# Optimization experiments

Measured on AMD Instinct MI355X. Metric: run time of the kernel, lower is better.

The kernel has to match this reference:

```python
import jax, jax.numpy as jnp
import numpy as np

B, L, D_IN, D, DEPTH, H = 1, 4095, 1536, 768, 4, 12
HD = D // H
FFN = 4 * D
GRID = 128
TILE = 256
SEGMENTS = (1024, 2048, 4096, 8192, 16384)
RATIOS = (1, 2, 4, 8, 16)
EPS = 1e-5
NEG = -1e9


def _sincos_1d(d, pos):
    omega = 1.0 / (10000.0 ** (np.arange(d // 2, dtype=np.float64) / (d / 2.0)))
    out = np.einsum('m,d->md', pos.reshape(-1).astype(np.float64), omega)
    return np.concatenate([np.sin(out), np.cos(out)], axis=1)


def _pos_embed_2d(d, g):
    # MAE-style 2d sincos grid; row index = coords[...,0], col = coords[...,1]
    gw, gh = np.meshgrid(np.arange(g, dtype=np.float64), np.arange(g, dtype=np.float64))
    emb_h = _sincos_1d(d // 2, gw)
    emb_w = _sincos_1d(d // 2, gh)
    pe = np.concatenate([emb_h, emb_w], axis=1)  # [g*g, d]
    return np.concatenate([np.zeros((1, d)), pe], axis=0).astype(np.float32)  # cls row


def setup_inputs() -> dict:
    key = jax.random.key(0)
    ks = jax.random.split(key, 16)
    n = lambda k, sh: 0.02 * jax.random.normal(k, sh, jnp.float32)
    x = jax.random.normal(ks[0], (B, L, D_IN), jnp.float32)
    coords = jax.random.uniform(ks[1], (B, L, 2), jnp.float32, 0.0, float(GRID * TILE))
    return {
        'x': x,
        'coords': coords,
        'pos_embed': jnp.asarray(_pos_embed_2d(D, GRID)),
        'cls_token': n(ks[2], (1, 1, D)),
        'patch_w': n(ks[3], (D_IN, D)),
        'patch_b': jnp.zeros((D,), jnp.float32),
        'ln1_g': jnp.ones((DEPTH, D), jnp.float32),
        'ln1_b': jnp.zeros((DEPTH, D), jnp.float32),
        'wq': n(ks[4], (DEPTH, D, D)), 'bq': jnp.zeros((DEPTH, D), jnp.float32),
        'wk': n(ks[5], (DEPTH, D, D)), 'bk': jnp.zeros((DEPTH, D), jnp.float32),
        'wv': n(ks[6], (DEPTH, D, D)), 'bv': jnp.zeros((DEPTH, D), jnp.float32),
        'wo': n(ks[7], (DEPTH, D, D)), 'bo': jnp.zeros((DEPTH, D), jnp.float32),
        'ln2_g': jnp.ones((DEPTH, D), jnp.float32),
        'ln2_b': jnp.zeros((DEPTH, D), jnp.float32),
        'w1': n(ks[8], (DEPTH, D, FFN)), 'b1': jnp.zeros((DEPTH, FFN), jnp.float32),
        'w2': n(ks[9], (DEPTH, FFN, D)), 'b2': jnp.zeros((DEPTH, D), jnp.float32),
        'enc_ln_g': jnp.ones((D,), jnp.float32),
        'enc_ln_b': jnp.zeros((D,), jnp.float32),
        'norm_g': jnp.ones((D,), jnp.float32),
        'norm_b': jnp.zeros((D,), jnp.float32),
    }


def _ln(t, g, b):
    m = t.mean(-1, keepdims=True)
    v = ((t - m) ** 2).mean(-1, keepdims=True)
    return (t - m) * jax.lax.rsqrt(v + EPS) * g + b


def _branch(q, k, v, w, r):
    # One LongNet dilated branch: segments of length w, per-head dilation r.
    Bq, S, Hh, hd = q.shape
    Lp = ((S + w - 1) // w) * w
    pad = Lp - S
    if pad:
        q = jnp.pad(q, ((0, 0), (0, pad), (0, 0), (0, 0)))
        k = jnp.pad(k, ((0, 0), (0, pad), (0, 0), (0, 0)))
        v = jnp.pad(v, ((0, 0), (0, pad), (0, 0), (0, 0)))
    n = Lp // w
    m = w // r
    # head-dependent offset subsampling (offset = head % r)
    idx = (jnp.arange(Hh) % r)[:, None] + r * jnp.arange(m)[None, :]  # [H, m]

    def seg(t):
        t = t.reshape(Bq, n, w, Hh, hd).transpose(0, 1, 3, 2, 4)  # [B,n,H,w,hd]
        return jnp.take_along_axis(t, idx[None, None, :, :, None], axis=3)  # [B,n,H,m,hd]

    qs, ks, vs = seg(q), seg(k), seg(v)
    valid = (jnp.arange(n)[:, None, None] * w + idx[None]) < S  # [n,H,m] key validity
    s = jnp.einsum('bnhqd,bnhkd->bnhqk', qs, ks)
    s = jnp.where(valid[None, :, :, None, :], s, NEG)
    lse_s = jax.scipy.special.logsumexp(s, axis=-1)              # [B,n,H,m]
    o_s = jnp.einsum('bnhqk,bnhkd->bnhqd', jax.nn.softmax(s, axis=-1), vs)
    hix = jnp.arange(Hh)[:, None]
    out = jnp.zeros((Bq, n, Hh, w, hd), q.dtype).at[:, :, hix, idx].set(o_s)
    lse = jnp.full((Bq, n, Hh, w), NEG, q.dtype).at[:, :, hix, idx].set(lse_s)
    out = out.transpose(0, 1, 3, 2, 4).reshape(Bq, Lp, Hh, hd)[:, :S]
    lse = lse.transpose(0, 1, 3, 2).reshape(Bq, Lp, Hh)[:, :S]
    return out, lse


def _forward(x, coords, pos_embed, cls_token, patch_w, patch_b, ln1_g, ln1_b,
             wq, bq, wk, bk, wv, bv, wo, bo, ln2_g, ln2_b, w1, b1, w2, b2,
             enc_ln_g, enc_ln_b, norm_g, norm_b):
    h = x @ patch_w + patch_b  # PatchEmbed (norm_layer=None -> Identity)
    c = jnp.floor(coords / TILE)
    pos = (c[..., 0] * GRID + c[..., 1]).astype(jnp.int32) + 1  # [B,L]
    h = h + pos_embed[pos]
    cls = jnp.broadcast_to(cls_token + pos_embed[0], (h.shape[0], 1, D))
    h = jnp.concatenate([cls, h], axis=1)  # [B, S, D], S = L+1
    S = h.shape[1]

    def layer(hcur, p):
        g1, bb1, wq_, bq_, wk_, bk_, wv_, bv_, wo_, bo_, g2, bb2, wf1, bf1, wf2, bf2 = p
        t = _ln(hcur, g1, bb1)
        q = (t @ wq_ + bq_).reshape(B, S, H, HD) * (HD ** -0.5)
        k = (t @ wk_ + bk_).reshape(B, S, H, HD)
        v = (t @ wv_ + bv_).reshape(B, S, H, HD)
        outs, lses = [], []
        for w_, r_ in zip(SEGMENTS, RATIOS):
            o, l = _branch(q, k, v, w_, r_)
            outs.append(o)
            lses.append(l)
        # LongNet combine: branches weighted by their softmax denominators
        wts = jax.nn.softmax(jnp.stack(lses), axis=0)  # [nb,B,S,H]
        attn = (wts[..., None] * jnp.stack(outs)).sum(0).reshape(B, S, D)
        hcur = hcur + attn @ wo_ + bo_
        t = _ln(hcur, g2, bb2)
        hcur = hcur + jax.nn.gelu(t @ wf1 + bf1) @ wf2 + bf2
        return hcur, None

    h, _ = jax.lax.scan(layer, h, (ln1_g, ln1_b, wq, bq, wk, bk, wv, bv,
                                   wo, bo, ln2_g, ln2_b, w1, b1, w2, b2))
    h = _ln(h, enc_ln_g, enc_ln_b)  # encoder final LN (normalize_before)
    h = _ln(h, norm_g, norm_b)      # module self.norm
    return h[:, 0]                  # cls token (global_pool=False)


def reference(x, coords, pos_embed, cls_token, patch_w, patch_b, ln1_g, ln1_b,
              wq, bq, wk, bk, wv, bv, wo, bo, ln2_g, ln2_b, w1, b1, w2, b2,
              enc_ln_g, enc_ln_b, norm_g, norm_b):
    return _forward(x, coords, pos_embed, cls_token, patch_w, patch_b, ln1_g, ln1_b,
                    wq, bq, wk, bk, wv, bv, wo, bo, ln2_g, ln2_b, w1, b1, w2, b2,
                    enc_ln_g, enc_ln_b, norm_g, norm_b)
```

## Files before the change

### kernel.cpp

```cpp
#include <hip/hip_runtime.h>
#include <hip/hip_bf16.h>
#include <math.h>
#include <stdint.h>

#define S_LEN 4096
#define L_LEN 4095
#define DIN   1536
#define DM    768
#define NHEAD 12
#define HDIM  64
#define FFND  3072
#define NEGV  (-1e9f)
#define EPS   1e-5f

typedef unsigned short u16;
typedef unsigned int   u32;
typedef short short8 __attribute__((ext_vector_type(8)));
typedef float f32x4 __attribute__((ext_vector_type(4)));
typedef float f32x16 __attribute__((ext_vector_type(16)));
typedef int i32x2 __attribute__((ext_vector_type(2)));

__device__ __forceinline__ u16 f2b(float f) {
    union { float f; u32 u; } x; x.f = f;
    u32 r = (x.u + 0x7FFF + ((x.u >> 16) & 1)) >> 16;
    return (u16)r;
}
__device__ __forceinline__ float b2f(u16 v) {
    union { u32 u; float f; } x; x.u = ((u32)v) << 16;
    return x.f;
}
__device__ __forceinline__ float gelu_tanh(float x) {
    float x3 = x * x * x;
    return 0.5f * x * (1.f + tanhf(0.7978845608f * (x + 0.044715f * x3)));
}
__device__ __forceinline__ float block_reduce_sum(float v, float* sbuf) {
#pragma unroll
    for (int o = 32; o > 0; o >>= 1) v += __shfl_down(v, o, 64);
    __syncthreads();
    if ((threadIdx.x & 63) == 0) sbuf[threadIdx.x >> 6] = v;
    __syncthreads();
    return sbuf[0] + sbuf[1] + sbuf[2] + sbuf[3];
}
__device__ __forceinline__ void gload16(const void* g, void* l) {
    __builtin_amdgcn_global_load_lds((const __attribute__((address_space(1))) void*)g,
                                     (__attribute__((address_space(3))) void*)l,
                                     16, 0, 0);
}
__device__ __forceinline__ void lds_barrier() {
    asm volatile("s_waitcnt lgkmcnt(0)" ::: "memory");
    __builtin_amdgcn_s_barrier();
    __builtin_amdgcn_sched_barrier(0);
}

template <int BM, int BN>
__device__ __forceinline__ void gemm_bt(
    const u16* __restrict__ A, const u16* __restrict__ Bt,
    const float* __restrict__ bias, const float* __restrict__ res,
    float* __restrict__ outf, u16* __restrict__ outb,
    int M, int N, int K, float scale, int dogelu, int bx, int by)
{
    constexpr int MI = BM / 32;
    constexpr int NI = BN / 32;
    constexpr int AI = BM / 32;
    constexpr int BI = BN / 32;
    __shared__ u16 As[BM * 64];
    __shared__ u16 Bs[BN * 64];
    const int tid = threadIdx.x, wv = tid >> 6, l = tid & 63;
    const int bm = by * BM, bn = bx * BN;
    const int wm = wv >> 1, wn = wv & 1;

    f32x4 acc[MI][NI];
#pragma unroll
    for (int i = 0; i < MI; ++i)
#pragma unroll
        for (int j = 0; j < NI; ++j) acc[i][j] = (f32x4){0.f, 0.f, 0.f, 0.f};

    for (int k0 = 0; k0 < K; k0 += 64) {
#pragma unroll
        for (int i = 0; i < AI; ++i) {
            int row = (wv * AI + i) * 8 + (l >> 3);
            int col = ((l & 7) ^ (row & 7)) * 8;
            int grow = bm + row; if (grow > M - 1) grow = M - 1;
            gload16(A + (size_t)grow * K + k0 + col, &As[(wv * AI + i) * 512]);
        }
#pragma unroll
        for (int i = 0; i < BI; ++i) {
            int row = (wv * BI + i) * 8 + (l >> 3);
            int col = ((l & 7) ^ (row & 7)) * 8;
            gload16(Bt + (size_t)(bn + row) * K + k0 + col, &Bs[(wv * BI + i) * 512]);
        }
        __syncthreads();
#pragma unroll
        for (int kc = 0; kc < 2; ++kc) {
            short8 a[MI], b[NI];
#pragma unroll
            for (int mi = 0; mi < MI; ++mi) {
                int row = wm * (BM / 2) + mi * 16 + (l & 15);
                int off = ((l >> 4) * 16 + kc * 64) ^ ((row & 7) << 4);
                a[mi] = *(const short8*)&As[(row * 128 + off) >> 1];
            }
#pragma unroll
            for (int ni = 0; ni < NI; ++ni) {
                int row = wn * (BN / 2) + ni * 16 + (l & 15);
                int off = ((l >> 4) * 16 + kc * 64) ^ ((row & 7) << 4);
                b[ni] = *(const short8*)&Bs[(row * 128 + off) >> 1];
            }
#pragma unroll
            for (int mi = 0; mi < MI; ++mi)
#pragma unroll
                for (int ni = 0; ni < NI; ++ni)
                    acc[mi][ni] = __builtin_amdgcn_mfma_f32_16x16x32_bf16(
                        a[mi], b[ni], acc[mi][ni], 0, 0, 0);
        }
        __syncthreads();
    }
#pragma unroll
    for (int mi = 0; mi < MI; ++mi) {
#pragma unroll
        for (int rg = 0; rg < 4; ++rg) {
            int row = bm + wm * (BM / 2) + mi * 16 + (l >> 4) * 4 + rg;
            if (row >= M) continue;
#pragma unroll
            for (int ni = 0; ni < NI; ++ni) {
                int col = bn + wn * (BN / 2) + ni * 16 + (l & 15);
                float v = (acc[mi][ni][rg] + bias[col]) * scale;
                if (dogelu) v = gelu_tanh(v);
                if (res) v += res[(size_t)row * N + col];
                if (outf) outf[(size_t)row * N + col] = v;
                if (outb) outb[(size_t)row * N + col] = f2b(v);
            }
        }
    }
}

__global__ __launch_bounds__(256) void gemm128_kernel(
    const u16* __restrict__ A, const u16* __restrict__ Bt,
    const float* __restrict__ bias, const float* __restrict__ res,
    float* __restrict__ outf, u16* __restrict__ outb,
    int M, int N, int K, float scale, int dogelu)
{
    gemm_bt<128, 128>(A, Bt, bias, res, outf, outb, M, N, K, scale, dogelu,
                      blockIdx.x, blockIdx.y);
}
__global__ __launch_bounds__(256) void gemm6464_kernel(
    const u16* __restrict__ A, const u16* __restrict__ Bt,
    const float* __restrict__ bias, const float* __restrict__ res,
    float* __restrict__ outf, u16* __restrict__ outb,
    int M, int N, int K, float scale, int dogelu)
{
    gemm_bt<64, 64>(A, Bt, bias, res, outf, outb, M, N, K, scale, dogelu,
                    blockIdx.x, blockIdx.y);
}
__global__ __launch_bounds__(256) void qkv_kernel(
    const u16* __restrict__ t,
    const u16* __restrict__ wqT, const u16* __restrict__ wkT, const u16* __restrict__ wvT,
    const float* __restrict__ bq, const float* __restrict__ bk, const float* __restrict__ bv,
    u16* __restrict__ q, u16* __restrict__ k, u16* __restrict__ v)
{
    int z = blockIdx.z;
    const u16* B = (z == 0) ? wqT : (z == 1) ? wkT : wvT;
    const float* bias = (z == 0) ? bq : (z == 1) ? bk : bv;
    u16* C = (z == 0) ? q : (z == 1) ? k : v;
    float scale = (z == 0) ? 0.125f * 1.4426950408889634f : 1.0f;
    gemm_bt<128, 128>(t, B, bias, nullptr, nullptr, C, S_LEN, DM, DM, scale, 0,
                      blockIdx.x, blockIdx.y);
}

__global__ __launch_bounds__(256) void transpose_cvt(
    const float* __restrict__ s0, const float* __restrict__ s1,
    const float* __restrict__ s2, const float* __restrict__ s3,
    u16* __restrict__ dst, int K, int N)
{
    int z = blockIdx.z;
    const float* src = (z == 0) ? s0 : (z == 1) ? s1 : (z == 2) ? s2 : s3;
    u16* d = dst + (size_t)z * K * N;
    __shared__ float tile[64][65];
    const int t = threadIdx.x;
    const int tk = blockIdx.y * 64, tn = blockIdx.x * 64;
    const int r0 = t >> 4, c0 = (t & 15) * 4;
#pragma unroll
    for (int i = 0; i < 4; ++i) {
        const float* sp = &src[(size_t)(tk + r0 + i * 16) * N + tn + c0];
        tile[r0 + i * 16][c0 + 0] = sp[0];
        tile[r0 + i * 16][c0 + 1] = sp[1];
        tile[r0 + i * 16][c0 + 2] = sp[2];
        tile[r0 + i * 16][c0 + 3] = sp[3];
    }
    __syncthreads();
#pragma unroll
    for (int i = 0; i < 4; ++i) {
        int nr = r0 + i * 16;
        u32 lo = (u32)f2b(tile[c0 + 0][nr]) | ((u32)f2b(tile[c0 + 1][nr]) << 16);
        u32 hi = (u32)f2b(tile[c0 + 2][nr]) | ((u32)f2b(tile[c0 + 3][nr]) << 16);
        *(uint2*)&d[(size_t)(tn + nr) * K + tk + c0] = make_uint2(lo, hi);
    }
}

__global__ __launch_bounds__(256) void prep_weights(
    const float* __restrict__ wq, const float* __restrict__ wk,
    const float* __restrict__ wv, const float* __restrict__ wo,
    const float* __restrict__ w1, const float* __restrict__ w2,
    u16* __restrict__ wTdd, u16* __restrict__ w1T, u16* __restrict__ w2T)
{
    __shared__ float tile[64][65];
    const int id = blockIdx.x;
    const float* src; u16* dst; int K, N, tk64, tn64;
    if (id < 576) {
        int z = id / 144, rm = id % 144;
        src = (z == 0) ? wq : (z == 1) ? wk : (z == 2) ? wv : wo;
        dst = wTdd + (size_t)z * DM * DM;
        K = DM; N = DM; tk64 = rm / 12; tn64 = rm % 12;
    } else if (id < 1152) {
        int rm = id - 576;
        src = w1; dst = w1T; K = DM; N = FFND; tk64 = rm / 48; tn64 = rm % 48;
    } else {
        int rm = id - 1152;
        src = w2; dst = w2T; K = FFND; N = DM; tk64 = rm / 12; tn64 = rm % 12;
    }
    const int t = threadIdx.x;
    const int tk = tk64 * 64, tn = tn64 * 64;
    const int r0 = t >> 4, c0 = (t & 15) * 4;
#pragma unroll
    for (int i = 0; i < 4; ++i) {
        const float* sp = &src[(size_t)(tk + r0 + i * 16) * N + tn + c0];
        tile[r0 + i * 16][c0 + 0] = sp[0];
        tile[r0 + i * 16][c0 + 1] = sp[1];
        tile[r0 + i * 16][c0 + 2] = sp[2];
        tile[r0 + i * 16][c0 + 3] = sp[3];
    }
    __syncthreads();
#pragma unroll
    for (int i = 0; i < 4; ++i) {
        int nr = r0 + i * 16;
        u32 lo = (u32)f2b(tile[c0 + 0][nr]) | ((u32)f2b(tile[c0 + 1][nr]) << 16);
        u32 hi = (u32)f2b(tile[c0 + 2][nr]) | ((u32)f2b(tile[c0 + 3][nr]) << 16);
        *(uint2*)&dst[(size_t)(tn + nr) * K + tk + c0] = make_uint2(lo, hi);
    }
}

__global__ __launch_bounds__(256) void cvt_bf16_kernel(
    const float* __restrict__ x, u16* __restrict__ xb, int n4)
{
    int stride = gridDim.x * 256;
    for (int i = blockIdx.x * 256 + threadIdx.x; i < n4; i += stride) {
        float4 v = ((const float4*)x)[i];
        u32 lo = (u32)f2b(v.x) | ((u32)f2b(v.y) << 16);
        u32 hi = (u32)f2b(v.z) | ((u32)f2b(v.w) << 16);
        ((uint2*)xb)[i] = make_uint2(lo, hi);
    }
}

__global__ __launch_bounds__(192) void ln_kernel(
    const float* __restrict__ in, u16* __restrict__ out,
    const float* __restrict__ g, const float* __restrict__ b)
{
    __shared__ float sA[3], sB[3];
    const int s = blockIdx.x, tid = threadIdx.x;
    float4 x = ((const float4*)(in + (size_t)s * DM))[tid];
    float sum = x.x + x.y + x.z + x.w;
#pragma unroll
    for (int o = 32; o > 0; o >>= 1) sum += __shfl_down(sum, o, 64);
    if ((tid & 63) == 0) sA[tid >> 6] = sum;
    __syncthreads();
    float m = (sA[0] + sA[1] + sA[2]) * (1.f / DM);
    float dx = x.x - m, dy = x.y - m, dz = x.z - m, dw = x.w - m;
    float vs = dx * dx + dy * dy + dz * dz + dw * dw;
#pragma unroll
    for (int o = 32; o > 0; o >>= 1) vs += __shfl_down(vs, o, 64);
    if ((tid & 63) == 0) sB[tid >> 6] = vs;
    __syncthreads();
    float rs = rsqrtf((sB[0] + sB[1] + sB[2]) * (1.f / DM) + EPS);
    float4 gv = ((const float4*)g)[tid];
    float4 bv = ((const float4*)b)[tid];
    u32 lo = (u32)f2b(dx * rs * gv.x + bv.x) | ((u32)f2b(dy * rs * gv.y + bv.y) << 16);
    u32 hi = (u32)f2b(dz * rs * gv.z + bv.z) | ((u32)f2b(dw * rs * gv.w + bv.w) << 16);
    ((uint2*)(out + (size_t)s * DM))[tid] = make_uint2(lo, hi);
}

__global__ __launch_bounds__(256) void posadd_kernel(
    float* __restrict__ h, const float* __restrict__ coords,
    const float* __restrict__ pe, const float* __restrict__ cls)
{
    const int s = blockIdx.x;
    const int tid = threadIdx.x;
    if (s == 0) {
        for (int c = tid; c < DM; c += 256) h[c] = cls[c] + pe[c];
    } else {
        float c0 = floorf(coords[(size_t)(s - 1) * 2 + 0] * (1.f / 256.f));
        float c1 = floorf(coords[(size_t)(s - 1) * 2 + 1] * (1.f / 256.f));
        int pos = (int)(c0 * 128.f + c1) + 1;
        float* hr = h + (size_t)s * DM;
        const float* pr = pe + (size_t)pos * DM;
        for (int c = tid; c < DM; c += 256) hr[c] += pr[c];
    }
}

__global__ __launch_bounds__(256, 3) void attn_kernel(
    const u16* __restrict__ qb, const u16* __restrict__ kbuf, const u16* __restrict__ vb,
    u16* __restrict__ obuf, u16* __restrict__ tp, float* __restrict__ lse)
{
    __shared__ u16 Vt[2][64 * 64];
    __shared__ float dbuf[4][32];

    const int tid = threadIdx.x, wv = tid >> 6, l = tid & 63;
    const int lq = l & 31, lh = l >> 5;
    const int bid = blockIdx.x;
    int b, half = 0, qtile, head, seg = 0;
    if (bid < 768) {
        b = 0; int i = bid; half = i & 1; qtile = (i >> 1) & 7;
        int rest = i >> 4; head = rest % 12; seg = rest / 12;
    } else if (bid < 1152) {
        b = 1; int i = bid - 768; half = i & 1; qtile = (i >> 1) & 7;
        int rest = i >> 4; head = rest % 12; seg = rest / 12;
    } else if (bid < 1344) {
        b = 2; int i = bid - 1152; half = i & 1; qtile = (i >> 1) & 7;
        head = i >> 4;
    } else if (bid < 1392) {
        b = 3; int i = bid - 1344; qtile = i & 3; head = i >> 2;
    } else {
        b = 4; int i = bid - 1392; qtile = i & 1; head = i >> 1;
    }
    const int slot = (b < 3) ? b * 2 + half : 3 + b;
    const int r = 1 << b;
    const int w = 1024 << b;
    const int keyoff = (b < 3) ? half * 512 : 0;
    const int ntiles = (b == 4) ? 4 : 8;
    const size_t base = (size_t)seg * w + (head & (r - 1));
    const int q0 = qtile * 128 + wv * 32;
    const size_t kstep = (size_t)r * DM;

    const size_t sq_l = base + (size_t)r * (q0 + lq);
    const u16* qp = qb + sq_l * DM + head * 64 + lh * 8;
    short8 qf[4];
#pragma unroll
    for (int s = 0; s < 4; ++s) qf[s] = *(const short8*)(qp + s * 16);

    const u16* kp = kbuf + (base + (size_t)r * (keyoff + lq)) * DM + head * 64 + lh * 8;
    const int c = tid & 7, pp = tid >> 3;
    const u16* vsrc = vb + (base + (size_t)r * (keyoff + 2 * pp)) * DM + head * 64 + c * 8;

#define VPACK(dstbuf, A8, B8) do {                                          \
    _Pragma("unroll") for (int j = 0; j < 8; ++j) {                         \
        int i_ = (j + c) & 7; int hd_ = c * 8 + i_;                         \
        u32 val_ = (u32)(u16)(A8)[i_] | ((u32)(u16)(B8)[i_] << 16);         \
        int byte_ = hd_ * 128 + ((pp * 4) ^ (i_ << 4));                     \
        *(u32*)&Vt[dstbuf][byte_ >> 1] = val_; } } while (0)

    f32x16 oacc0 = {0.f,0.f,0.f,0.f,0.f,0.f,0.f,0.f,0.f,0.f,0.f,0.f,0.f,0.f,0.f,0.f};
    f32x16 oacc1 = oacc0;
    float mw = -INFINITY, dl = 0.f;

    short8 van = *(const short8*)vsrc;
    short8 vbn = *(const short8*)(vsrc + kstep);
    VPACK(0, van, vbn);
    van = *(const short8*)(vsrc + 64 * kstep);
    vbn = *(const short8*)(vsrc + 65 * kstep);
    short8 kf[8];
#pragma unroll
    for (int s = 0; s < 4; ++s) {
        kf[s]     = *(const short8*)(kp + s * 16);
        kf[4 + s] = *(const short8*)(kp + 32 * kstep + s * 16);
    }
    lds_barrier();

    for (int t = 0; t < ntiles; ++t) {
        const int curb = t & 1;
        f32x16 s0 = {0.f,0.f,0.f,0.f,0.f,0.f,0.f,0.f,0.f,0.f,0.f,0.f,0.f,0.f,0.f,0.f};
        f32x16 s1 = s0;
#pragma unroll
        for (int s = 0; s < 4; ++s)
            s0 = __builtin_amdgcn_mfma_f32_32x32x16_bf16(kf[s], qf[s], s0, 0, 0, 0);
#pragma unroll
        for (int s = 0; s < 4; ++s)
            s1 = __builtin_amdgcn_mfma_f32_32x32x16_bf16(kf[4 + s], qf[s], s1, 0, 0, 0);

        if (t + 1 < ntiles) {
            const u16* kn = kp + (size_t)(t + 1) * 64 * kstep;
#pragma unroll
            for (int s = 0; s < 4; ++s) {
                kf[s]     = *(const short8*)(kn + s * 16);
                kf[4 + s] = *(const short8*)(kn + 32 * kstep + s * 16);
            }
        }

        float pm[16];
#pragma unroll
        for (int i = 0; i < 16; ++i) pm[i] = fmaxf(s0[i], s1[i]);
#pragma unroll
        for (int i = 0; i < 8; ++i) pm[i] = fmaxf(pm[i], pm[i + 8]);
#pragma unroll
        for (int i = 0; i < 4; ++i) pm[i] = fmaxf(pm[i], pm[i + 4]);
        float mloc = fmaxf(fmaxf(pm[0], pm[1]), fmaxf(pm[2], pm[3]));
        if (__any(mloc > mw + 8.f)) {
            float mn = mloc;
#pragma unroll
            for (int o = 1; o < 64; o <<= 1) mn = fmaxf(mn, __shfl_xor(mn, o, 64));
            float al = exp2f(mw - mn);
            mw = mn;
            dl *= al;
#pragma unroll
            for (int i = 0; i < 16; ++i) { oacc0[i] *= al; oacc1[i] *= al; }
        }
        float ds = 0.f;
#pragma unroll
        for (int i = 0; i < 16; ++i) { s0[i] = exp2f(s0[i] - mw); ds += s0[i]; }
#pragma unroll
        for (int i = 0; i < 16; ++i) { s1[i] = exp2f(s1[i] - mw); ds += s1[i]; }
        ds += __shfl_xor(ds, 32, 64);
        dl += ds;

        if (t + 1 < ntiles) VPACK(curb ^ 1, van, vbn);
        if (t + 2 < ntiles) {
            van = *(const short8*)(vsrc + (size_t)(t + 2) * 64 * kstep);
            vbn = *(const short8*)(vsrc + ((size_t)(t + 2) * 64 + 1) * kstep);
        }

#pragma unroll
        for (int kb2 = 0; kb2 < 2; ++kb2) {
            u32 wd[8];
#pragma unroll
            for (int j = 0; j < 8; ++j) {
                float lo = (kb2 == 0) ? s0[2 * j] : s1[2 * j];
                float hi = (kb2 == 0) ? s0[2 * j + 1] : s1[2 * j + 1];
                asm("v_cvt_pk_bf16_f32 %0, %1, %2" : "=v"(wd[j]) : "v"(lo), "v"(hi));
            }
#pragma unroll
            for (int ks2 = 0; ks2 < 2; ++ks2) {
                i32x2 X = __builtin_amdgcn_permlane32_swap(
                    (int)wd[ks2 * 4 + 0], (int)wd[ks2 * 4 + 2], false, false);
                i32x2 Y = __builtin_amdgcn_permlane32_swap(
                    (int)wd[ks2 * 4 + 1], (int)wd[ks2 * 4 + 3], false, false);
                union { u32 u[4]; short8 s; } pk;
                pk.u[0] = (u32)X[0]; pk.u[1] = (u32)Y[0];
                pk.u[2] = (u32)X[1]; pk.u[3] = (u32)Y[1];
                const int tt = kb2 * 2 + ks2;
#pragma unroll
                for (int hg = 0; hg < 2; ++hg) {
                    int row = hg * 32 + lq;
                    int byteoff = row * 128 + ((lh * 16 + tt * 32) ^ ((row & 7) << 4));
                    short8 vf = *(const short8*)&Vt[curb][byteoff >> 1];
                    if (hg == 0)
                        oacc0 = __builtin_amdgcn_mfma_f32_32x32x16_bf16(pk.s, vf, oacc0, 0, 0, 0);
                    else
                        oacc1 = __builtin_amdgcn_mfma_f32_32x32x16_bf16(pk.s, vf, oacc1, 0, 0, 0);
                }
            }
        }
        lds_barrier();
    }

    if (l < 32) dbuf[wv][lq] = dl;
    u16* ob = (slot == 7) ? tp : obuf + (size_t)slot * S_LEN * DM;
    float* lse_b = lse + (size_t)slot * S_LEN * NHEAD;
    if (l < 32) lse_b[sq_l * NHEAD + head] = mw + log2f(dl);
#pragma unroll
    for (int reg = 0; reg < 16; ++reg) {
        int qloc = (reg & 3) + 8 * (reg >> 2) + 4 * lh;
        float invd = 1.f / dbuf[wv][qloc];
        size_t sq = base + (size_t)r * (q0 + qloc);
        u16* orow = ob + sq * DM + head * 64;
        u32 pk2;
        float v0 = oacc0[reg] * invd, v1 = oacc1[reg] * invd;
        asm("v_cvt_pk_bf16_f32 %0, %1, %2" : "=v"(pk2) : "v"(v0), "v"(v1));
        orow[lq]      = (u16)(pk2 & 0xffff);
        orow[32 + lq] = (u16)(pk2 >> 16);
    }
#undef VPACK
}

__global__ __launch_bounds__(192) void combine_kernel(
    const u16* __restrict__ obuf, const float* __restrict__ lse,
    u16* __restrict__ t)
{
    const int s = blockIdx.x;
    const int tid = threadIdx.x;
    const int c0 = tid * 4, head = c0 >> 6;
    const size_t SD = (size_t)S_LEN * DM;
    const size_t SN = (size_t)S_LEN * NHEAD;
    const bool v6 = ((s ^ head) & 7) == 0;
    const bool v7 = (s & 15) == head;
    float lv[8];
#pragma unroll
    for (int b = 0; b < 6; ++b)
        lv[b] = lse[b * SN + (size_t)s * NHEAD + head];
    lv[6] = v6 ? lse[6 * SN + (size_t)s * NHEAD + head] : NEGV;
    lv[7] = v7 ? lse[7 * SN + (size_t)s * NHEAD + head] : NEGV;
    float mx = lv[0];
#pragma unroll
    for (int b = 1; b < 8; ++b) mx = fmaxf(mx, lv[b]);
    float wsum = 0.f, o0 = 0.f, o1 = 0.f, o2 = 0.f, o3 = 0.f;
#pragma unroll
    for (int b = 0; b < 8; ++b) {
        bool valid = (b < 6) | (b == 6 && v6) | (b == 7 && v7);
        if (valid) {
            float wb = exp2f(lv[b] - mx);
            wsum += wb;
            const u16* src = (b == 7) ? t : obuf + (size_t)b * SD;
            uint2 u = *(const uint2*)(src + (size_t)s * DM + c0);
            o0 += wb * b2f((u16)(u.x & 0xffff));
            o1 += wb * b2f((u16)(u.x >> 16));
            o2 += wb * b2f((u16)(u.y & 0xffff));
            o3 += wb * b2f((u16)(u.y >> 16));
        }
    }
    float inv = 1.f / wsum;
    u32 lo = (u32)f2b(o0 * inv) | ((u32)f2b(o1 * inv) << 16);
    u32 hi = (u32)f2b(o2 * inv) | ((u32)f2b(o3 * inv) << 16);
    ((uint2*)(t + (size_t)s * DM))[tid] = make_uint2(lo, hi);
}

__global__ __launch_bounds__(256) void final_ln_kernel(
    const float* __restrict__ h,
    const float* __restrict__ g1, const float* __restrict__ b1,
    const float* __restrict__ g2, const float* __restrict__ b2,
    float* __restrict__ out)
{
    __shared__ float sbuf[4];
    const int tid = threadIdx.x;
    float x0 = h[tid], x1 = h[tid + 256], x2 = h[tid + 512];
    float m = block_reduce_sum(x0 + x1 + x2, sbuf) * (1.f / DM);
    float d0 = x0 - m, d1 = x1 - m, d2 = x2 - m;
    float var = block_reduce_sum(d0 * d0 + d1 * d1 + d2 * d2, sbuf) * (1.f / DM);
    float rs = rsqrtf(var + EPS);
    float y0 = d0 * rs * g1[tid]       + b1[tid];
    float y1 = d1 * rs * g1[tid + 256] + b1[tid + 256];
    float y2 = d2 * rs * g1[tid + 512] + b1[tid + 512];
    m = block_reduce_sum(y0 + y1 + y2, sbuf) * (1.f / DM);
    d0 = y0 - m; d1 = y1 - m; d2 = y2 - m;
    var = block_reduce_sum(d0 * d0 + d1 * d1 + d2 * d2, sbuf) * (1.f / DM);
    rs = rsqrtf(var + EPS);
    out[tid]       = d0 * rs * g2[tid]       + b2[tid];
    out[tid + 256] = d1 * rs * g2[tid + 256] + b2[tid + 256];
    out[tid + 512] = d2 * rs * g2[tid + 512] + b2[tid + 512];
}

extern "C" void kernel_launch(void* const* d_in, const int* in_sizes, int n_in,
                              void* d_out, int out_size, void* d_ws, size_t ws_size,
                              hipStream_t stream)
{
    (void)in_sizes; (void)n_in; (void)out_size; (void)ws_size;
    const float* x        = (const float*)d_in[0];
    const float* coords   = (const float*)d_in[1];
    const float* pos_emb  = (const float*)d_in[2];
    const float* cls_tok  = (const float*)d_in[3];
    const float* patch_w  = (const float*)d_in[4];
    const float* patch_b  = (const float*)d_in[5];
    const float* ln1_g    = (const float*)d_in[6];
    const float* ln1_b    = (const float*)d_in[7];
    const float* wq       = (const float*)d_in[8];
    const float* bq       = (const float*)d_in[9];
    const float* wk       = (const float*)d_in[10];
    const float* bk       = (const float*)d_in[11];
    const float* wv       = (const float*)d_in[12];
    const float* bv       = (const float*)d_in[13];
    const float* wo       = (const float*)d_in[14];
    const float* bo       = (const float*)d_in[15];
    const float* ln2_g    = (const float*)d_in[16];
    const float* ln2_b    = (const float*)d_in[17];
    const float* w1       = (const float*)d_in[18];
    const float* b1       = (const float*)d_in[19];
    const float* w2       = (const float*)d_in[20];
    const float* b2       = (const float*)d_in[21];
    const float* enc_g    = (const float*)d_in[22];
    const float* enc_b    = (const float*)d_in[23];
    const float* norm_g   = (const float*)d_in[24];
    const float* norm_b   = (const float*)d_in[25];
    float* out = (float*)d_out;

    const size_t SD = (size_t)S_LEN * DM;
    const size_t DD = (size_t)DM * DM;
    const size_t DF = (size_t)DM * FFND;
    const size_t SN = (size_t)S_LEN * NHEAD;

    char* p = (char*)d_ws;
    float* h   = (float*)p;              p += SD * 4;
    u16* t     = (u16*)p;                p += SD * 2;
    u16* qb    = (u16*)p;                p += SD * 2;
    u16* kb    = (u16*)p;                p += SD * 2;
    u16* vb    = (u16*)p;                p += SD * 2;
    float* lse = (float*)p;              p += 8 * SN * 4;
    u16* obuf  = (u16*)p;                p += 7 * SD * 2;
    u16* ffn   = obuf;
    u16* xb    = obuf;
    u16* pwT   = (u16*)p;                p += (size_t)DIN * DM * 2;
    u16* wTdd  = (u16*)p;                p += 4 * DD * 2;
    u16* w1T   = (u16*)p;                p += DF * 2;
    u16* w2T   = (u16*)p;                p += DF * 2;

    cvt_bf16_kernel<<<2048, 256, 0, stream>>>(x, xb, (L_LEN * DIN) / 4);
    transpose_cvt<<<dim3(DM / 64, DIN / 64, 1), 256, 0, stream>>>(
        patch_w, patch_w, patch_w, patch_w, pwT, DIN, DM);
    gemm6464_kernel<<<dim3(DM / 64, 64), 256, 0, stream>>>(
        xb, pwT, patch_b, nullptr, h + DM, nullptr, L_LEN, DM, DIN, 1.f, 0);
    posadd_kernel<<<S_LEN, 256, 0, stream>>>(h, coords, pos_emb, cls_tok);

    for (int l = 0; l < 4; ++l) {
        const size_t lDD = (size_t)l * DD;
        const size_t lDF = (size_t)l * DF;
        prep_weights<<<1728, 256, 0, stream>>>(
            wq + lDD, wk + lDD, wv + lDD, wo + lDD, w1 + lDF, w2 + lDF,
            wTdd, w1T, w2T);

        ln_kernel<<<S_LEN, 192, 0, stream>>>(h, t, ln1_g + l * DM, ln1_b + l * DM);
        qkv_kernel<<<dim3(6, 32, 3), 256, 0, stream>>>(
            t, wTdd, wTdd + DD, wTdd + 2 * DD,
            bq + l * DM, bk + l * DM, bv + l * DM, qb, kb, vb);
        attn_kernel<<<1416, 256, 0, stream>>>(qb, kb, vb, obuf, t, lse);
        combine_kernel<<<S_LEN, 192, 0, stream>>>(obuf, lse, t);
        gemm6464_kernel<<<dim3(12, 64), 256, 0, stream>>>(
            t, wTdd + 3 * DD, bo + l * DM, h, h, nullptr, S_LEN, DM, DM, 1.f, 0);
        ln_kernel<<<S_LEN, 192, 0, stream>>>(h, t, ln2_g + l * DM, ln2_b + l * DM);
        gemm128_kernel<<<dim3(24, 32), 256, 0, stream>>>(
            t, w1T, b1 + (size_t)l * FFND, nullptr, nullptr, ffn,
            S_LEN, FFND, DM, 1.f, 1);
        gemm6464_kernel<<<dim3(12, 64), 256, 0, stream>>>(
            ffn, w2T, b2 + l * DM, h, h, nullptr, S_LEN, DM, FFND, 1.f, 0);
    }
    final_ln_kernel<<<1, 256, 0, stream>>>(h, enc_g, enc_b, norm_g, norm_b, out);
}
```

Measured before the change: 1.104 ms.

## Pre-transpose V per dilation branch and load V fragments directly from global

Adds a vtrans kernel that writes V in a per-branch, per-head transposed layout, so the attention kernel can load the PV-MMA operands straight into registers. This removes the in-kernel LDS transpose, the double buffer and the per-tile barriers. The row-sum broadcast now uses a shuffle instead of shared memory, and MFMA sections are wrapped in s_setprio. Separately, the 64x64 GEMMs (patch, out-proj, FFN2) become 128x64 tiles. The cost is an extra kernel launch per layer, about 5x the V size in extra workspace and global traffic, and fewer blocks for the N=768 GEMMs.

```diff
diff --git a/kernel.cpp b/kernel.cpp
--- a/kernel.cpp
+++ b/kernel.cpp
@@ -46,11 +46,6 @@
                                      (__attribute__((address_space(3))) void*)l,
                                      16, 0, 0);
 }
-__device__ __forceinline__ void lds_barrier() {
-    asm volatile("s_waitcnt lgkmcnt(0)" ::: "memory");
-    __builtin_amdgcn_s_barrier();
-    __builtin_amdgcn_sched_barrier(0);
-}
 
 template <int BM, int BN>
 __device__ __forceinline__ void gemm_bt(
@@ -142,14 +137,14 @@
     gemm_bt<128, 128>(A, Bt, bias, res, outf, outb, M, N, K, scale, dogelu,
                       blockIdx.x, blockIdx.y);
 }
-__global__ __launch_bounds__(256) void gemm6464_kernel(
+__global__ __launch_bounds__(256) void gemm12864_kernel(
     const u16* __restrict__ A, const u16* __restrict__ Bt,
     const float* __restrict__ bias, const float* __restrict__ res,
     float* __restrict__ outf, u16* __restrict__ outb,
     int M, int N, int K, float scale, int dogelu)
 {
-    gemm_bt<64, 64>(A, Bt, bias, res, outf, outb, M, N, K, scale, dogelu,
-                    blockIdx.x, blockIdx.y);
+    gemm_bt<128, 64>(A, Bt, bias, res, outf, outb, M, N, K, scale, dogelu,
+                     blockIdx.x, blockIdx.y);
 }
 __global__ __launch_bounds__(256) void qkv_kernel(
     const u16* __restrict__ t,
@@ -238,6 +233,48 @@
     }
 }
 
+__global__ __launch_bounds__(256) void vtrans_kernel(
+    const u16* __restrict__ vb, u16* __restrict__ vtb)
+{
+    __shared__ u16 tile[64 * 64];
+    const int t = threadIdx.x;
+    const int iblk = blockIdx.x;
+    const int head = blockIdx.y;
+    const int b = blockIdx.z;
+    const int r = 1 << b;
+    const int sr = 4096 >> b;
+    const int idx0 = iblk * 64;
+    const int c = idx0 / sr;
+    const int q0 = idx0 - c * sr;
+    {
+        const int i = t >> 2, hc = (t & 3) * 16;
+        const int pos = c + r * (q0 + i);
+        const u16* src = vb + (size_t)pos * DM + head * 64 + hc;
+        short8 a = *(const short8*)src;
+        short8 d = *(const short8*)(src + 8);
+        const int sw = (i & 7) << 4;
+        *(short8*)((char*)tile + i * 128 + ((hc * 2) ^ sw)) = a;
+        *(short8*)((char*)tile + i * 128 + (((hc * 2) + 16) ^ sw)) = d;
+    }
+    __syncthreads();
+#pragma unroll
+    for (int it = 0; it < 2; ++it) {
+        int wi = t + it * 256;
+        int hd = wi >> 3, grp = wi & 7;
+        u16 v[8];
+#pragma unroll
+        for (int j = 0; j < 8; ++j)
+            v[j] = *(const u16*)((char*)tile + (grp * 8 + j) * 128 + ((hd * 2) ^ (j << 4)));
+        uint4 o;
+        o.x = (u32)v[0] | ((u32)v[1] << 16);
+        o.y = (u32)v[2] | ((u32)v[3] << 16);
+        o.z = (u32)v[4] | ((u32)v[5] << 16);
+        o.w = (u32)v[6] | ((u32)v[7] << 16);
+        u16* dst = vtb + (((size_t)b * NHEAD + head) * 64 + hd) * S_LEN + idx0 + grp * 8;
+        *(uint4*)dst = o;
+    }
+}
+
 __global__ __launch_bounds__(256) void cvt_bf16_kernel(
     const float* __restrict__ x, u16* __restrict__ xb, int n4)
 {
@@ -296,13 +333,11 @@
 }
 
 __global__ __launch_bounds__(256, 3) void attn_kernel(
-    const u16* __restrict__ qb, const u16* __restrict__ kbuf, const u16* __restrict__ vb,
+    const u16* __restrict__ qb, const u16* __restrict__ kbuf,
+    const u16* __restrict__ vtb,
     u16* __restrict__ obuf, u16* __restrict__ tp, float* __restrict__ lse)
 {
-    __shared__ u16 Vt[2][64 * 64];
-    __shared__ float dbuf[4][32];
-
-    const int tid = threadIdx.x, wv = tid >> 6, l = tid & 63;
+    const int tid = threadIdx.x, l = tid & 63;
     const int lq = l & 31, lh = l >> 5;
     const int bid = blockIdx.x;
     int b, half = 0, qtile, head, seg = 0;
@@ -320,9 +355,11 @@
     } else {
         b = 4; int i = bid - 1392; qtile = i & 1; head = i >> 1;
     }
+    const int wv = tid >> 6;
     const int slot = (b < 3) ? b * 2 + half : 3 + b;
     const int r = 1 << b;
     const int w = 1024 << b;
+    const int sr = 4096 >> b;
     const int keyoff = (b < 3) ? half * 512 : 0;
     const int ntiles = (b == 4) ? 4 : 8;
     const size_t base = (size_t)seg * w + (head & (r - 1));
@@ -336,43 +373,37 @@
     for (int s = 0; s < 4; ++s) qf[s] = *(const short8*)(qp + s * 16);
 
     const u16* kp = kbuf + (base + (size_t)r * (keyoff + lq)) * DM + head * 64 + lh * 8;
-    const int c = tid & 7, pp = tid >> 3;
-    const u16* vsrc = vb + (base + (size_t)r * (keyoff + 2 * pp)) * DM + head * 64 + c * 8;
-
-#define VPACK(dstbuf, A8, B8) do {                                          \
-    _Pragma("unroll") for (int j = 0; j < 8; ++j) {                         \
-        int i_ = (j + c) & 7; int hd_ = c * 8 + i_;                         \
-        u32 val_ = (u32)(u16)(A8)[i_] | ((u32)(u16)(B8)[i_] << 16);         \
-        int byte_ = hd_ * 128 + ((pp * 4) ^ (i_ << 4));                     \
-        *(u32*)&Vt[dstbuf][byte_ >> 1] = val_; } } while (0)
+    const u16* vr0 = vtb + (((size_t)b * NHEAD + head) * 64 + lq) * S_LEN
+                   + (head & (r - 1)) * sr + seg * 1024 + keyoff + lh * 8;
+    const u16* vr1 = vr0 + (size_t)32 * S_LEN;
 
     f32x16 oacc0 = {0.f,0.f,0.f,0.f,0.f,0.f,0.f,0.f,0.f,0.f,0.f,0.f,0.f,0.f,0.f,0.f};
     f32x16 oacc1 = oacc0;
     float mw = -INFINITY, dl = 0.f;
 
-    short8 van = *(const short8*)vsrc;
-    short8 vbn = *(const short8*)(vsrc + kstep);
-    VPACK(0, van, vbn);
-    van = *(const short8*)(vsrc + 64 * kstep);
-    vbn = *(const short8*)(vsrc + 65 * kstep);
-    short8 kf[8];
+    short8 kf[8], vf0[4], vf1[4];
 #pragma unroll
     for (int s = 0; s < 4; ++s) {
         kf[s]     = *(const short8*)(kp + s * 16);
         kf[4 + s] = *(const short8*)(kp + 32 * kstep + s * 16);
     }
-    lds_barrier();
+#pragma unroll
+    for (int tt = 0; tt < 4; ++tt) {
+        vf0[tt] = *(const short8*)(vr0 + tt * 16);
+        vf1[tt] = *(const short8*)(vr1 + tt * 16);
+    }
 
     for (int t = 0; t < ntiles; ++t) {
-        const int curb = t & 1;
         f32x16 s0 = {0.f,0.f,0.f,0.f,0.f,0.f,0.f,0.f,0.f,0.f,0.f,0.f,0.f,0.f,0.f,0.f};
         f32x16 s1 = s0;
+        __builtin_amdgcn_s_setprio(1);
 #pragma unroll
         for (int s = 0; s < 4; ++s)
             s0 = __builtin_amdgcn_mfma_f32_32x32x16_bf16(kf[s], qf[s], s0, 0, 0, 0);
 #pragma unroll
         for (int s = 0; s < 4; ++s)
             s1 = __builtin_amdgcn_mfma_f32_32x32x16_bf16(kf[4 + s], qf[s], s1, 0, 0, 0);
+        __builtin_amdgcn_s_setprio(0);
 
         if (t + 1 < ntiles) {
             const u16* kn = kp + (size_t)(t + 1) * 64 * kstep;
@@ -409,12 +440,7 @@
         ds += __shfl_xor(ds, 32, 64);
         dl += ds;
 
-        if (t + 1 < ntiles) VPACK(curb ^ 1, van, vbn);
-        if (t + 2 < ntiles) {
-            van = *(const short8*)(vsrc + (size_t)(t + 2) * 64 * kstep);
-            vbn = *(const short8*)(vsrc + ((size_t)(t + 2) * 64 + 1) * kstep);
-        }
-
+        __builtin_amdgcn_s_setprio(1);
 #pragma unroll
         for (int kb2 = 0; kb2 < 2; ++kb2) {
             u32 wd[8];
@@ -434,29 +460,31 @@
                 pk.u[0] = (u32)X[0]; pk.u[1] = (u32)Y[0];
                 pk.u[2] = (u32)X[1]; pk.u[3] = (u32)Y[1];
                 const int tt = kb2 * 2 + ks2;
-#pragma unroll
-                for (int hg = 0; hg < 2; ++hg) {
-                    int row = hg * 32 + lq;
-                    int byteoff = row * 128 + ((lh * 16 + tt * 32) ^ ((row & 7) << 4));
-                    short8 vf = *(const short8*)&Vt[curb][byteoff >> 1];
-                    if (hg == 0)
-                        oacc0 = __builtin_amdgcn_mfma_f32_32x32x16_bf16(pk.s, vf, oacc0, 0, 0, 0);
-                    else
-                        oacc1 = __builtin_amdgcn_mfma_f32_32x32x16_bf16(pk.s, vf, oacc1, 0, 0, 0);
-                }
+                oacc0 = __builtin_amdgcn_mfma_f32_32x32x16_bf16(pk.s, vf0[tt], oacc0, 0, 0, 0);
+                oacc1 = __builtin_amdgcn_mfma_f32_32x32x16_bf16(pk.s, vf1[tt], oacc1, 0, 0, 0);
             }
         }
-        lds_barrier();
-    }
-
-    if (l < 32) dbuf[wv][lq] = dl;
+        __builtin_amdgcn_s_setprio(0);
+
+        if (t + 1 < ntiles) {
+            const u16* vn0 = vr0 + (t + 1) * 64;
+            const u16* vn1 = vr1 + (t + 1) * 64;
+#pragma unroll
+            for (int tt = 0; tt < 4; ++tt) {
+                vf0[tt] = *(const short8*)(vn0 + tt * 16);
+                vf1[tt] = *(const short8*)(vn1 + tt * 16);
+            }
+        }
+    }
+
     u16* ob = (slot == 7) ? tp : obuf + (size_t)slot * S_LEN * DM;
     float* lse_b = lse + (size_t)slot * S_LEN * NHEAD;
     if (l < 32) lse_b[sq_l * NHEAD + head] = mw + log2f(dl);
 #pragma unroll
     for (int reg = 0; reg < 16; ++reg) {
         int qloc = (reg & 3) + 8 * (reg >> 2) + 4 * lh;
-        float invd = 1.f / dbuf[wv][qloc];
+        float dq = __shfl(dl, qloc, 64);
+        float invd = 1.f / dq;
         size_t sq = base + (size_t)r * (q0 + qloc);
         u16* orow = ob + sq * DM + head * 64;
         u32 pk2;
@@ -465,7 +493,6 @@
         orow[lq]      = (u16)(pk2 & 0xffff);
         orow[32 + lq] = (u16)(pk2 >> 16);
     }
-#undef VPACK
 }
 
 __global__ __launch_bounds__(192) void combine_kernel(
@@ -578,6 +605,7 @@
     u16* qb    = (u16*)p;                p += SD * 2;
     u16* kb    = (u16*)p;                p += SD * 2;
     u16* vb    = (u16*)p;                p += SD * 2;
+    u16* vtb   = (u16*)p;                p += 5 * SD * 2;
     float* lse = (float*)p;              p += 8 * SN * 4;
     u16* obuf  = (u16*)p;                p += 7 * SD * 2;
     u16* ffn   = obuf;
@@ -590,7 +618,7 @@
     cvt_bf16_kernel<<<2048, 256, 0, stream>>>(x, xb, (L_LEN * DIN) / 4);
     transpose_cvt<<<dim3(DM / 64, DIN / 64, 1), 256, 0, stream>>>(
         patch_w, patch_w, patch_w, patch_w, pwT, DIN, DM);
-    gemm6464_kernel<<<dim3(DM / 64, 64), 256, 0, stream>>>(
+    gemm12864_kernel<<<dim3(12, 32), 256, 0, stream>>>(
         xb, pwT, patch_b, nullptr, h + DM, nullptr, L_LEN, DM, DIN, 1.f, 0);
     posadd_kernel<<<S_LEN, 256, 0, stream>>>(h, coords, pos_emb, cls_tok);
 
@@ -605,15 +633,16 @@
         qkv_kernel<<<dim3(6, 32, 3), 256, 0, stream>>>(
             t, wTdd, wTdd + DD, wTdd + 2 * DD,
             bq + l * DM, bk + l * DM, bv + l * DM, qb, kb, vb);
-        attn_kernel<<<1416, 256, 0, stream>>>(qb, kb, vb, obuf, t, lse);
+        vtrans_kernel<<<dim3(64, NHEAD, 5), 256, 0, stream>>>(vb, vtb);
+        attn_kernel<<<1416, 256, 0, stream>>>(qb, kb, vtb, obuf, t, lse);
         combine_kernel<<<S_LEN, 192, 0, stream>>>(obuf, lse, t);
-        gemm6464_kernel<<<dim3(12, 64), 256, 0, stream>>>(
+        gemm12864_kernel<<<dim3(12, 32), 256, 0, stream>>>(
             t, wTdd + 3 * DD, bo + l * DM, h, h, nullptr, S_LEN, DM, DM, 1.f, 0);
         ln_kernel<<<S_LEN, 192, 0, stream>>>(h, t, ln2_g + l * DM, ln2_b + l * DM);
         gemm128_kernel<<<dim3(24, 32), 256, 0, stream>>>(
             t, w1T, b1 + (size_t)l * FFND, nullptr, nullptr, ffn,
             S_LEN, FFND, DM, 1.f, 1);
-        gemm6464_kernel<<<dim3(12, 64), 256, 0, stream>>>(
+        gemm12864_kernel<<<dim3(12, 32), 256, 0, stream>>>(
             ffn, w2T, b2 + l * DM, h, h, nullptr, S_LEN, DM, FFND, 1.f, 0);
     }
     final_ln_kernel<<<1, 256, 0, stream>>>(h, enc_g, enc_b, norm_g, norm_b, out);
```

After: 1.306 ms. 18.3% more time.

## Compute only the CLS row in the last layer after attention

Applied to the files above, without the earlier changes.

The output only needs the CLS token, so in the final layer attention, the output projection, LN2 and the FFN are computed for row 0 only. New kernels do this: a per-head CLS attention that combines the dilated branches, and a row GEMV for the projections. This removes most of the last layer's attention and GEMM work, and K/V are still computed in full for all rows. The risk is correctness if the branch validity and dilation logic for row 0 does not exactly match the full kernel's semantics.

```diff
diff --git a/kernel.cpp b/kernel.cpp
--- a/kernel.cpp
+++ b/kernel.cpp
@@ -507,6 +507,118 @@
     u32 lo = (u32)f2b(o0 * inv) | ((u32)f2b(o1 * inv) << 16);
     u32 hi = (u32)f2b(o2 * inv) | ((u32)f2b(o3 * inv) << 16);
     ((uint2*)(t + (size_t)s * DM))[tid] = make_uint2(lo, hi);
+}
+
+__global__ __launch_bounds__(256) void cls_attn_kernel(
+    const u16* __restrict__ qb, const u16* __restrict__ kb,
+    const u16* __restrict__ vb, u16* __restrict__ t)
+{
+    __shared__ float q0[64];
+    __shared__ float sc[1024];
+    __shared__ float red4[4];
+    __shared__ float po[256];
+    __shared__ float obr[5][64];
+    __shared__ float lseb[5];
+    const int head = blockIdx.x, tid = threadIdx.x;
+    if (tid < 64) q0[tid] = b2f(qb[head * 64 + tid]);
+    __syncthreads();
+
+    for (int b = 0; b < 5; ++b) {
+        const int r = 1 << b;
+        const bool valid = (head & (r - 1)) == 0;
+        if (!valid) {
+            if (tid == 0) lseb[b] = NEGV;
+            __syncthreads();
+            continue;
+        }
+        const int nv = (b < 3) ? 1024 : (b == 3 ? 512 : 256);
+        const int nit = nv >> 8;
+        float smax = -1e30f;
+        for (int it = 0; it < nit; ++it) {
+            int j = tid + it * 256;
+            const u16* kp = kb + (size_t)j * r * DM + head * 64;
+            float acc = 0.f;
+#pragma unroll
+            for (int d8 = 0; d8 < 8; ++d8) {
+                short8 kv = *(const short8*)(kp + d8 * 8);
+#pragma unroll
+                for (int jj = 0; jj < 8; ++jj)
+                    acc += q0[d8 * 8 + jj] * b2f((u16)kv[jj]);
+            }
+            sc[j] = acc;
+            smax = fmaxf(smax, acc);
+        }
+#pragma unroll
+        for (int o = 32; o > 0; o >>= 1) smax = fmaxf(smax, __shfl_xor(smax, o, 64));
+        if ((tid & 63) == 0) red4[tid >> 6] = smax;
+        __syncthreads();
+        float bm = fmaxf(fmaxf(red4[0], red4[1]), fmaxf(red4[2], red4[3]));
+        __syncthreads();
+        float ssum = 0.f;
+        for (int it = 0; it < nit; ++it) {
+            int j = tid + it * 256;
+            float pv = exp2f(sc[j] - bm);
+            sc[j] = pv;
+            ssum += pv;
+        }
+#pragma unroll
+        for (int o = 32; o > 0; o >>= 1) ssum += __shfl_xor(ssum, o, 64);
+        if ((tid & 63) == 0) red4[tid >> 6] = ssum;
+        __syncthreads();
+        float dsum = red4[0] + red4[1] + red4[2] + red4[3];
+        __syncthreads();
+        const int hd = tid & 63, ch = tid >> 6;
+        const int cl = nv >> 2;
+        float o = 0.f;
+        for (int j = ch * cl; j < (ch + 1) * cl; ++j)
+            o += sc[j] * b2f(vb[(size_t)j * r * DM + head * 64 + hd]);
+        po[tid] = o;
+        __syncthreads();
+        if (tid < 64)
+            obr[b][tid] = (po[tid] + po[tid + 64] + po[tid + 128] + po[tid + 192]) / dsum;
+        if (tid == 0) lseb[b] = bm + log2f(dsum);
+        __syncthreads();
+    }
+    if (tid < 64) {
+        float mx = -1e30f;
+#pragma unroll
+        for (int b = 0; b < 5; ++b) mx = fmaxf(mx, lseb[b]);
+        float ws = 0.f, ov = 0.f;
+#pragma unroll
+        for (int b = 0; b < 5; ++b) {
+            float lv = lseb[b];
+            if (lv > -1e8f) {
+                float wb = exp2f(lv - mx);
+                ws += wb;
+                ov += wb * obr[b][tid];
+            }
+        }
+        t[head * 64 + tid] = f2b(ov / ws);
+    }
+}
+
+__global__ __launch_bounds__(256) void row_gemv_kernel(
+    const u16* __restrict__ x, const u16* __restrict__ wT,
+    const float* __restrict__ bias, const float* __restrict__ res,
+    float* __restrict__ outf, u16* __restrict__ outb, int K, int dogelu)
+{
+    __shared__ float xs[3072];
+    const int tid = threadIdx.x;
+    for (int i = tid; i < K; i += 256) xs[i] = b2f(x[i]);
+    __syncthreads();
+    const int n = blockIdx.x * 256 + tid;
+    const u16* wrow = wT + (size_t)n * K;
+    float acc = 0.f;
+    for (int k = 0; k < K; k += 8) {
+        short8 wv = *(const short8*)(wrow + k);
+#pragma unroll
+        for (int j = 0; j < 8; ++j) acc += xs[k + j] * b2f((u16)wv[j]);
+    }
+    float v = acc + bias[n];
+    if (dogelu) v = gelu_tanh(v);
+    if (res) v += res[n];
+    if (outf) outf[n] = v;
+    if (outb) outb[n] = f2b(v);
 }
 
 __global__ __launch_bounds__(256) void final_ln_kernel(
@@ -605,16 +717,28 @@
         qkv_kernel<<<dim3(6, 32, 3), 256, 0, stream>>>(
             t, wTdd, wTdd + DD, wTdd + 2 * DD,
             bq + l * DM, bk + l * DM, bv + l * DM, qb, kb, vb);
-        attn_kernel<<<1416, 256, 0, stream>>>(qb, kb, vb, obuf, t, lse);
-        combine_kernel<<<S_LEN, 192, 0, stream>>>(obuf, lse, t);
-        gemm6464_kernel<<<dim3(12, 64), 256, 0, stream>>>(
-            t, wTdd + 3 * DD, bo + l * DM, h, h, nullptr, S_LEN, DM, DM, 1.f, 0);
-        ln_kernel<<<S_LEN, 192, 0, stream>>>(h, t, ln2_g + l * DM, ln2_b + l * DM);
-        gemm128_kernel<<<dim3(24, 32), 256, 0, stream>>>(
-            t, w1T, b1 + (size_t)l * FFND, nullptr, nullptr, ffn,
-            S_LEN, FFND, DM, 1.f, 1);
-        gemm6464_kernel<<<dim3(12, 64), 256, 0, stream>>>(
-            ffn, w2T, b2 + l * DM, h, h, nullptr, S_LEN, DM, FFND, 1.f, 0);
+
+        if (l < 3) {
+            attn_kernel<<<1416, 256, 0, stream>>>(qb, kb, vb, obuf, t, lse);
+            combine_kernel<<<S_LEN, 192, 0, stream>>>(obuf, lse, t);
+            gemm6464_kernel<<<dim3(12, 64), 256, 0, stream>>>(
+                t, wTdd + 3 * DD, bo + l * DM, h, h, nullptr, S_LEN, DM, DM, 1.f, 0);
+            ln_kernel<<<S_LEN, 192, 0, stream>>>(h, t, ln2_g + l * DM, ln2_b + l * DM);
+            gemm128_kernel<<<dim3(24, 32), 256, 0, stream>>>(
+                t, w1T, b1 + (size_t)l * FFND, nullptr, nullptr, ffn,
+                S_LEN, FFND, DM, 1.f, 1);
+            gemm6464_kernel<<<dim3(12, 64), 256, 0, stream>>>(
+                ffn, w2T, b2 + l * DM, h, h, nullptr, S_LEN, DM, FFND, 1.f, 0);
+        } else {
+            cls_attn_kernel<<<NHEAD, 256, 0, stream>>>(qb, kb, vb, t);
+            row_gemv_kernel<<<3, 256, 0, stream>>>(
+                t, wTdd + 3 * DD, bo + l * DM, h, h, nullptr, DM, 0);
+            ln_kernel<<<1, 192, 0, stream>>>(h, t, ln2_g + l * DM, ln2_b + l * DM);
+            row_gemv_kernel<<<12, 256, 0, stream>>>(
+                t, w1T, b1 + (size_t)l * FFND, nullptr, nullptr, ffn, DM, 1);
+            row_gemv_kernel<<<3, 256, 0, stream>>>(
+                ffn, w2T, b2 + l * DM, h, h, nullptr, FFND, 0);
+        }
     }
     final_ln_kernel<<<1, 256, 0, stream>>>(h, enc_g, enc_b, norm_g, norm_b, out);
 }
```

New measurement: 1.233 ms. +11.7%, slower.
